# Kernel optimization log

Measured on AMD Instinct MI355X. Metric: run time of the kernel, lower is better.

Reference implementation:

```python
import jax, jax.numpy as jnp
import numpy as np

D_MODEL = 1024
NUM_HEADS = 16
D_K = D_MODEL // NUM_HEADS


def setup_inputs() -> dict:
    key = jax.random.key(0)
    ks = jax.random.split(key, 11)
    B, T = 4, 2048
    s = 1.0 / np.sqrt(D_MODEL)
    inp = {
        "query": jax.random.normal(ks[0], (B, T, D_MODEL), jnp.float32),
        "key": jax.random.normal(ks[1], (B, T, D_MODEL), jnp.float32),
        "value": jax.random.normal(ks[2], (B, T, D_MODEL), jnp.float32),
        "Wq": jax.random.uniform(ks[3], (D_MODEL, D_MODEL), jnp.float32, -s, s),
        "bq": jax.random.uniform(ks[4], (D_MODEL,), jnp.float32, -s, s),
        "Wk": jax.random.uniform(ks[5], (D_MODEL, D_MODEL), jnp.float32, -s, s),
        "bk": jax.random.uniform(ks[6], (D_MODEL,), jnp.float32, -s, s),
        "Wv": jax.random.uniform(ks[7], (D_MODEL, D_MODEL), jnp.float32, -s, s),
        "bv": jax.random.uniform(ks[8], (D_MODEL,), jnp.float32, -s, s),
        "Wo": jax.random.uniform(ks[9], (D_MODEL, D_MODEL), jnp.float32, -s, s),
        "bo": jax.random.uniform(ks[10], (D_MODEL,), jnp.float32, -s, s),
    }
    return inp


def _split_heads(x):
    B, T, _ = x.shape
    return x.reshape(B, T, NUM_HEADS, D_K).transpose(0, 2, 1, 3)  # (B,H,T,dk)


def reference(query, key, value, Wq, bq, Wk, bk, Wv, bv, Wo, bo):
    q = _split_heads(query @ Wq + bq)   # (B,H,Tq,dk)
    k = _split_heads(key @ Wk + bk)     # (B,H,Tk,dk)
    v = _split_heads(value @ Wv + bv)   # (B,H,Tk,dk)
    scale = 1.0 / jnp.sqrt(jnp.asarray(D_K, q.dtype))
    scores = jnp.einsum("bhqd,bhkd->bhqk", q, k) * scale
    weights = jax.nn.softmax(scores, axis=-1)
    attn = jnp.einsum("bhqk,bhkd->bhqd", weights, v)  # (B,H,Tq,dk)
    B, H, T, dk = attn.shape
    attn = attn.transpose(0, 2, 1, 3).reshape(B, T, H * dk)
    return attn @ Wo + bo
```

## Files before the change

kernel.cpp:

```cpp
#include <hip/hip_runtime.h>
#include <hip/hip_bf16.h>
#include <stdint.h>


typedef __bf16 bf16x8 __attribute__((ext_vector_type(8)));
typedef short  v4s    __attribute__((ext_vector_type(4)));
typedef float  f32x4  __attribute__((ext_vector_type(4)));

#define LOG2E 1.44269504088896340736f

static __device__ __forceinline__ uint32_t f2bf(float x) {
  uint32_t u = __float_as_uint(x);
  u += 0x7fffu + ((u >> 16) & 1u);
  return u >> 16;
}
#if __has_builtin(__builtin_amdgcn_cvt_pk_bf16_f32)
static __device__ __forceinline__ uint32_t pk2bf(float a, float b) {
  typedef __bf16 b2 __attribute__((ext_vector_type(2)));
  union { b2 v; uint32_t u; } x;
  x.v = __builtin_amdgcn_cvt_pk_bf16_f32(a, b);
  return x.u;
}
#else
static __device__ __forceinline__ uint32_t pk2bf(float a, float b) {
  return f2bf(a) | (f2bf(b) << 16);
}
#endif
static __device__ __forceinline__ void gl2lds16(const void* g, void* l) {
  __builtin_amdgcn_global_load_lds(
      (const __attribute__((address_space(1))) uint32_t*)g,
      (__attribute__((address_space(3))) uint32_t*)l, 16, 0, 0);
}

__global__ void convert_inputs(const float* __restrict__ q, const float* __restrict__ k,
                               const float* __restrict__ v, uint16_t* __restrict__ qo,
                               uint16_t* __restrict__ ko, uint16_t* __restrict__ vo) {
  const float* src = blockIdx.y == 0 ? q : (blockIdx.y == 1 ? k : v);
  uint16_t*    dst = blockIdx.y == 0 ? qo : (blockIdx.y == 1 ? ko : vo);
  size_t idx = ((size_t)blockIdx.x * 256 + threadIdx.x) * 8;
  float4 a = *(const float4*)(src + idx);
  float4 b = *(const float4*)(src + idx + 4);
  uint4 o;
  o.x = pk2bf(a.x, a.y); o.y = pk2bf(a.z, a.w);
  o.z = pk2bf(b.x, b.y); o.w = pk2bf(b.z, b.w);
  *(uint4*)(dst + idx) = o;
}

__global__ void transpose_weights(const float* __restrict__ Wq, const float* __restrict__ Wk,
                                  const float* __restrict__ Wv, const float* __restrict__ Wo,
                                  uint16_t* __restrict__ out) {
  __shared__ float t[32][33];
  const float* W = blockIdx.z == 0 ? Wq : blockIdx.z == 1 ? Wk : blockIdx.z == 2 ? Wv : Wo;
  uint16_t* O = out + (size_t)blockIdx.z * 1048576;
  int tx = threadIdx.x & 31, ty = threadIdx.x >> 5;
  int r0 = blockIdx.y * 32, c0 = blockIdx.x * 32;
#pragma unroll
  for (int i = 0; i < 4; i++) t[ty + i * 8][tx] = W[(size_t)(r0 + ty + i * 8) * 1024 + c0 + tx];
  __syncthreads();
#pragma unroll
  for (int i = 0; i < 4; i++)
    O[(size_t)(c0 + ty + i * 8) * 1024 + r0 + tx] = (uint16_t)f2bf(t[tx][ty + i * 8]);
}

static __device__ __forceinline__ void gemm_body(
    const uint16_t* __restrict__ A, const uint16_t* __restrict__ Bt,
    const float* __restrict__ bias, void* __restrict__ Cout,
    int N, int K, int mode, float oscale, int mBase, int nBase,
    uint16_t* __restrict__ lA, uint16_t* __restrict__ lB) {
  int tid = threadIdx.x, wave = tid >> 6, lane = tid & 63;
  int q = lane >> 4, c = lane & 15;
  int wrow = wave & 1, wcol = wave >> 1;
  f32x4 acc[4][4] = {};

  int swz = ((lane & 7) ^ (lane >> 3)) * 8;
  const uint16_t* gA = A + (size_t)(mBase + wave * 32 + (lane >> 3)) * K + swz;
  const uint16_t* gB = Bt + (size_t)(nBase + wave * 32 + (lane >> 3)) * K + swz;
  int cs = c & 7;

  for (int kt = 0; kt < K / 64; kt++) {
    __syncthreads();
    int k0 = kt * 64;
#pragma unroll
    for (int it = 0; it < 4; it++) {
      gl2lds16(gA + (size_t)(it * 8) * K + k0, &lA[(wave * 32 + it * 8) * 64]);
      gl2lds16(gB + (size_t)(it * 8) * K + k0, &lB[(wave * 32 + it * 8) * 64]);
    }
    __syncthreads();
#pragma unroll
    for (int kk = 0; kk < 2; kk++) {
      bf16x8 af[4], bfr[4];
#pragma unroll
      for (int i = 0; i < 4; i++)
        af[i] = *(const bf16x8*)&lA[(wrow * 64 + i * 16 + c) * 64 + ((kk * 4 + q) ^ cs) * 8];
#pragma unroll
      for (int j = 0; j < 4; j++)
        bfr[j] = *(const bf16x8*)&lB[(wcol * 64 + j * 16 + c) * 64 + ((kk * 4 + q) ^ cs) * 8];
#pragma unroll
      for (int i = 0; i < 4; i++)
#pragma unroll
        for (int j = 0; j < 4; j++)
          acc[i][j] = __builtin_amdgcn_mfma_f32_16x16x32_bf16(af[i], bfr[j], acc[i][j], 0, 0, 0);
    }
  }

  float bb[4];
#pragma unroll
  for (int j = 0; j < 4; j++) bb[j] = bias[nBase + wcol * 64 + j * 16 + c];

  if (mode == 0) {
    float* Co = (float*)Cout;
#pragma unroll
    for (int i = 0; i < 4; i++)
#pragma unroll
      for (int j = 0; j < 4; j++) {
        int row = mBase + wrow * 64 + i * 16 + q * 4;
        int col = nBase + wcol * 64 + j * 16 + c;
#pragma unroll
        for (int r = 0; r < 4; r++) Co[(size_t)(row + r) * N + col] = acc[i][j][r] + bb[j];
      }
  } else if (mode == 1) {
    uint16_t* Co = (uint16_t*)Cout;
#pragma unroll
    for (int i = 0; i < 4; i++)
#pragma unroll
      for (int j = 0; j < 4; j++) {
        int row = mBase + wrow * 64 + i * 16 + q * 4;
        int col = nBase + wcol * 64 + j * 16 + c;
#pragma unroll
        for (int r = 0; r < 4; r++)
          Co[(size_t)(row + r) * N + col] = (uint16_t)f2bf((acc[i][j][r] + bb[j]) * oscale);
      }
  } else {
    uint16_t* Co = (uint16_t*)Cout;
#pragma unroll
    for (int i = 0; i < 4; i++)
#pragma unroll
      for (int j = 0; j < 4; j++) {
        int n = nBase + wcol * 64 + j * 16 + c;
        int h = n >> 6, d = n & 63;
        int m = mBase + wrow * 64 + i * 16 + q * 4;
        int b = m >> 11, t = m & 2047;
        uint32_t lo = pk2bf(acc[i][j][0] + bb[j], acc[i][j][1] + bb[j]);
        uint32_t hi = pk2bf(acc[i][j][2] + bb[j], acc[i][j][3] + bb[j]);
        *(uint2*)(Co + (size_t)((b * 16 + h) * 64 + d) * 2048 + t) = make_uint2(lo, hi);
      }
  }
}

__global__ __launch_bounds__(256, 2)
void gemm_qkv(const uint16_t* __restrict__ qb, const uint16_t* __restrict__ kb,
              const uint16_t* __restrict__ vb, const uint16_t* __restrict__ Wtq,
              const uint16_t* __restrict__ Wtk, const uint16_t* __restrict__ Wtv,
              const float* __restrict__ bq, const float* __restrict__ bk,
              const float* __restrict__ bv, uint16_t* __restrict__ Qp,
              uint16_t* __restrict__ Kp, uint16_t* __restrict__ Vt, float cs) {
  __shared__ uint16_t lA[8192], lB[8192];
  int z = blockIdx.z;
  const uint16_t* A  = z == 0 ? qb : (z == 1 ? kb : vb);
  const uint16_t* Bt = z == 0 ? Wtq : (z == 1 ? Wtk : Wtv);
  const float* bias  = z == 0 ? bq : (z == 1 ? bk : bv);
  void* C            = z == 0 ? (void*)Qp : (z == 1 ? (void*)Kp : (void*)Vt);
  int mode   = z == 2 ? 2 : 1;
  float os   = z == 0 ? cs : 1.0f;
  gemm_body(A, Bt, bias, C, 1024, 1024, mode, os, blockIdx.y * 128, blockIdx.x * 128, lA, lB);
}

__global__ __launch_bounds__(256, 2)
void gemm_out(const uint16_t* __restrict__ A, const uint16_t* __restrict__ Bt,
              const float* __restrict__ bias, float* __restrict__ C) {
  __shared__ uint16_t lA[8192], lB[8192];
  gemm_body(A, Bt, bias, C, 1024, 1024, 0, 1.0f, blockIdx.y * 128, blockIdx.x * 128, lA, lB);
}

__global__ __launch_bounds__(256, 2)
void attn(const uint16_t* __restrict__ Qp, const uint16_t* __restrict__ Kp,
          const uint16_t* __restrict__ Vt, uint16_t* __restrict__ Ob) {
  __shared__ uint16_t lds[16384];
  int tid = threadIdx.x, wave = tid >> 6, lane = tid & 63;
  int q = lane >> 4, c = lane & 15;
  int cs = c & 7;

  int id = blockIdx.y * 16 + blockIdx.x;
  int wk = (id & 7) * 128 + (id >> 3);
  int qt = wk & 15, bh = wk >> 4;
  int b = bh >> 4, h = bh & 15;
  int qbase = qt * 128;
  int swz = ((lane & 7) ^ (lane >> 3)) * 8;

  {
    const uint16_t* gQ =
        Qp + (size_t)(b * 2048 + qbase + wave * 32 + (lane >> 3)) * 1024 + h * 64 + swz;
#pragma unroll
    for (int it = 0; it < 4; it++)
      gl2lds16(gQ + (size_t)(it * 8) * 1024, &lds[(wave * 32 + it * 8) * 64]);
  }
  __syncthreads();
  bf16x8 qf[2][2];
#pragma unroll
  for (int it = 0; it < 2; it++)
#pragma unroll
    for (int kk = 0; kk < 2; kk++)
      qf[it][kk] =
          *(const bf16x8*)&lds[(wave * 32 + it * 16 + c) * 64 + ((kk * 4 + q) ^ cs) * 8];
  __syncthreads();

  f32x4 o[4][2] = {};
  float rs0 = 0.f, rs1 = 0.f;

  const uint16_t* gK0 =
      Kp + (size_t)(b * 2048 + wave * 16 + (lane >> 3)) * 1024 + h * 64 + swz;
  const uint16_t* gV0 = Vt + (size_t)(bh * 64 + wave * 16 + (lane >> 3)) * 2048 + swz;

#pragma unroll
  for (int it = 0; it < 2; it++) {
    gl2lds16(gK0 + (size_t)(it * 8) * 1024, &lds[(wave * 16 + it * 8) * 64]);
    gl2lds16(gV0 + (size_t)(it * 8) * 2048, &lds[8192 + (wave * 16 + it * 8) * 64]);
  }

  for (int kt = 0; kt < 32; kt++) {
    int cur = kt & 1;
    __syncthreads();

    if (kt < 31) {
      int nb = (cur ^ 1) * 4096;
#pragma unroll
      for (int it = 0; it < 2; it++) {
        gl2lds16(gK0 + (size_t)((kt + 1) * 64 + it * 8) * 1024,
                 &lds[nb + (wave * 16 + it * 8) * 64]);
        gl2lds16(gV0 + (size_t)(it * 8) * 2048 + (kt + 1) * 64,
                 &lds[8192 + nb + (wave * 16 + it * 8) * 64]);
      }
    }

    const uint16_t* sKc = &lds[cur * 4096];
    const uint16_t* sVc = &lds[8192 + cur * 4096];

#pragma unroll
    for (int jt = 0; jt < 4; jt++) {
      bf16x8 a0 = *(const bf16x8*)&sKc[(jt * 16 + c) * 64 + (q ^ cs) * 8];
      bf16x8 a1 = *(const bf16x8*)&sKc[(jt * 16 + c) * 64 + ((4 + q) ^ cs) * 8];
      f32x4 s0 = __builtin_amdgcn_mfma_f32_16x16x32_bf16(a0, qf[0][0],
                                                         (f32x4){0.f, 0.f, 0.f, 0.f}, 0, 0, 0);
      s0 = __builtin_amdgcn_mfma_f32_16x16x32_bf16(a1, qf[0][1], s0, 0, 0, 0);
      f32x4 s1 = __builtin_amdgcn_mfma_f32_16x16x32_bf16(a0, qf[1][0],
                                                         (f32x4){0.f, 0.f, 0.f, 0.f}, 0, 0, 0);
      s1 = __builtin_amdgcn_mfma_f32_16x16x32_bf16(a1, qf[1][1], s1, 0, 0, 0);

      float p00 = __builtin_amdgcn_exp2f(s0[0]), p01 = __builtin_amdgcn_exp2f(s0[1]);
      float p02 = __builtin_amdgcn_exp2f(s0[2]), p03 = __builtin_amdgcn_exp2f(s0[3]);
      float p10 = __builtin_amdgcn_exp2f(s1[0]), p11 = __builtin_amdgcn_exp2f(s1[1]);
      float p12 = __builtin_amdgcn_exp2f(s1[2]), p13 = __builtin_amdgcn_exp2f(s1[3]);
      rs0 += (p00 + p01) + (p02 + p03);
      rs1 += (p10 + p11) + (p12 + p13);
      union { uint32_t u[2]; v4s s4; } pb0, pb1;
      pb0.u[0] = pk2bf(p00, p01); pb0.u[1] = pk2bf(p02, p03);
      pb1.u[0] = pk2bf(p10, p11); pb1.u[1] = pk2bf(p12, p13);

#pragma unroll
      for (int mt = 0; mt < 4; mt++) {
        v4s a = *(const v4s*)&sVc[(mt * 16 + c) * 64 + (((jt * 2 + (q >> 1)) ^ cs) * 8) +
                                  (q & 1) * 4];
        o[mt][0] = __builtin_amdgcn_mfma_f32_16x16x16bf16_1k(a, pb0.s4, o[mt][0], 0, 0, 0);
        o[mt][1] = __builtin_amdgcn_mfma_f32_16x16x16bf16_1k(a, pb1.s4, o[mt][1], 0, 0, 0);
      }
    }
  }

  rs0 += __shfl_xor(rs0, 16); rs0 += __shfl_xor(rs0, 32);
  rs1 += __shfl_xor(rs1, 16); rs1 += __shfl_xor(rs1, 32);
  float l[2] = {rs0, rs1};

#pragma unroll
  for (int it = 0; it < 2; it++) {
    float inv = 1.0f / l[it];
    size_t trow = (size_t)(b * 2048 + qbase + wave * 32 + it * 16 + c) * 1024 + h * 64;
#pragma unroll
    for (int mt = 0; mt < 4; mt++) {
      uint32_t lo = pk2bf(o[mt][it][0] * inv, o[mt][it][1] * inv);
      uint32_t hi = pk2bf(o[mt][it][2] * inv, o[mt][it][3] * inv);
      *(uint2*)(Ob + trow + mt * 16 + q * 4) = make_uint2(lo, hi);
    }
  }
}

extern "C" void kernel_launch(void* const* d_in, const int* in_sizes, int n_in,
                              void* d_out, int out_size, void* d_ws, size_t ws_size,
                              hipStream_t stream) {
  (void)in_sizes; (void)n_in; (void)out_size; (void)ws_size;
  const float* query = (const float*)d_in[0];
  const float* key_  = (const float*)d_in[1];
  const float* value = (const float*)d_in[2];
  const float* Wq = (const float*)d_in[3]; const float* bq = (const float*)d_in[4];
  const float* Wk = (const float*)d_in[5]; const float* bk = (const float*)d_in[6];
  const float* Wv = (const float*)d_in[7]; const float* bv = (const float*)d_in[8];
  const float* Wo = (const float*)d_in[9]; const float* bo = (const float*)d_in[10];

  const size_t SZ = (size_t)8192 * 1024;
  uint16_t* buf0 = (uint16_t*)d_ws;
  uint16_t* buf1 = buf0 + SZ;
  uint16_t* buf2 = buf1 + SZ;
  uint16_t* buf3 = buf2 + SZ;
  uint16_t* wts  = buf3 + SZ;
  uint16_t* Wtq = wts;
  uint16_t* Wtk = wts + 1048576;
  uint16_t* Wtv = wts + 2097152;
  uint16_t* Wto = wts + 3145728;
  uint16_t* Kp  = wts + 4194304;
  uint16_t* Vt  = Kp + SZ;

  const float Cs = 0.125f * LOG2E;

  convert_inputs<<<dim3(4096, 3), 256, 0, stream>>>(query, key_, value, buf0, buf1, buf2);
  transpose_weights<<<dim3(32, 32, 4), 256, 0, stream>>>(Wq, Wk, Wv, Wo, wts);
  gemm_qkv<<<dim3(8, 64, 3), 256, 0, stream>>>(buf0, buf1, buf2, Wtq, Wtk, Wtv,
                                               bq, bk, bv, buf3, Kp, Vt, Cs);
  attn<<<dim3(16, 64), 256, 0, stream>>>(buf3, Kp, Vt, buf2);
  gemm_out<<<dim3(8, 64), 256, 0, stream>>>(buf2, Wto, bo, (float*)d_out);
}
```

Baseline: 355.1 us.

## Widen attention blocks to 256 queries, XCD-swizzle GEMM tiles, add MFMA priority hints

The attention kernel now runs 512-thread blocks covering 256 query rows, so each K/V tile loaded into LDS is shared by twice as many queries. Each wave now loads only 8 rows per K/V tile. Both GEMM kernels remap block indices so neighbouring row tiles land on the same XCD, to improve L2 reuse of the A operand. s_setprio is raised around the MFMA sections of the attention inner loop so matrix work from one wave can overlap exp and convert work from others. The tighter launch bound of 512 threads with 4 blocks per CU lowers the per-thread register budget, which may cause spills in the attention kernel.

```diff
diff --git a/kernel.cpp b/kernel.cpp
--- a/kernel.cpp
+++ b/kernel.cpp
@@ -155,24 +155,32 @@
               const float* __restrict__ bv, uint16_t* __restrict__ Qp,
               uint16_t* __restrict__ Kp, uint16_t* __restrict__ Vt, float cs) {
   __shared__ uint16_t lA[8192], lB[8192];
-  int z = blockIdx.z;
+  int id = blockIdx.x + (blockIdx.y << 3) + (blockIdx.z << 9);
+  int xcd = id & 7, j = id >> 3;
+  int by = xcd * 8 + (j & 7);
+  int bx = (j >> 3) & 7;
+  int z  = j >> 6;
   const uint16_t* A  = z == 0 ? qb : (z == 1 ? kb : vb);
   const uint16_t* Bt = z == 0 ? Wtq : (z == 1 ? Wtk : Wtv);
   const float* bias  = z == 0 ? bq : (z == 1 ? bk : bv);
   void* C            = z == 0 ? (void*)Qp : (z == 1 ? (void*)Kp : (void*)Vt);
   int mode   = z == 2 ? 2 : 1;
   float os   = z == 0 ? cs : 1.0f;
-  gemm_body(A, Bt, bias, C, 1024, 1024, mode, os, blockIdx.y * 128, blockIdx.x * 128, lA, lB);
+  gemm_body(A, Bt, bias, C, 1024, 1024, mode, os, by * 128, bx * 128, lA, lB);
 }
 
 __global__ __launch_bounds__(256, 2)
 void gemm_out(const uint16_t* __restrict__ A, const uint16_t* __restrict__ Bt,
               const float* __restrict__ bias, float* __restrict__ C) {
   __shared__ uint16_t lA[8192], lB[8192];
-  gemm_body(A, Bt, bias, C, 1024, 1024, 0, 1.0f, blockIdx.y * 128, blockIdx.x * 128, lA, lB);
-}
-
-__global__ __launch_bounds__(256, 2)
+  int id = blockIdx.x + (blockIdx.y << 3);
+  int xcd = id & 7, j = id >> 3;
+  int by = xcd * 8 + (j & 7);
+  int bx = j >> 3;
+  gemm_body(A, Bt, bias, C, 1024, 1024, 0, 1.0f, by * 128, bx * 128, lA, lB);
+}
+
+__global__ __launch_bounds__(512, 4)
 void attn(const uint16_t* __restrict__ Qp, const uint16_t* __restrict__ Kp,
           const uint16_t* __restrict__ Vt, uint16_t* __restrict__ Ob) {
   __shared__ uint16_t lds[16384];
@@ -180,11 +188,11 @@
   int q = lane >> 4, c = lane & 15;
   int cs = c & 7;
 
-  int id = blockIdx.y * 16 + blockIdx.x;
-  int wk = (id & 7) * 128 + (id >> 3);
-  int qt = wk & 15, bh = wk >> 4;
+  int id = blockIdx.y * 8 + blockIdx.x;
+  int wk = (id & 7) * 64 + (id >> 3);
+  int qt = wk & 7, bh = wk >> 3;
   int b = bh >> 4, h = bh & 15;
-  int qbase = qt * 128;
+  int qbase = qt * 256;
   int swz = ((lane & 7) ^ (lane >> 3)) * 8;
 
   {
@@ -208,14 +216,11 @@
   float rs0 = 0.f, rs1 = 0.f;
 
   const uint16_t* gK0 =
-      Kp + (size_t)(b * 2048 + wave * 16 + (lane >> 3)) * 1024 + h * 64 + swz;
-  const uint16_t* gV0 = Vt + (size_t)(bh * 64 + wave * 16 + (lane >> 3)) * 2048 + swz;
-
-#pragma unroll
-  for (int it = 0; it < 2; it++) {
-    gl2lds16(gK0 + (size_t)(it * 8) * 1024, &lds[(wave * 16 + it * 8) * 64]);
-    gl2lds16(gV0 + (size_t)(it * 8) * 2048, &lds[8192 + (wave * 16 + it * 8) * 64]);
-  }
+      Kp + (size_t)(b * 2048 + wave * 8 + (lane >> 3)) * 1024 + h * 64 + swz;
+  const uint16_t* gV0 = Vt + (size_t)(bh * 64 + wave * 8 + (lane >> 3)) * 2048 + swz;
+
+  gl2lds16(gK0, &lds[(wave * 8) * 64]);
+  gl2lds16(gV0, &lds[8192 + (wave * 8) * 64]);
 
   for (int kt = 0; kt < 32; kt++) {
     int cur = kt & 1;
@@ -223,13 +228,8 @@
 
     if (kt < 31) {
       int nb = (cur ^ 1) * 4096;
-#pragma unroll
-      for (int it = 0; it < 2; it++) {
-        gl2lds16(gK0 + (size_t)((kt + 1) * 64 + it * 8) * 1024,
-                 &lds[nb + (wave * 16 + it * 8) * 64]);
-        gl2lds16(gV0 + (size_t)(it * 8) * 2048 + (kt + 1) * 64,
-                 &lds[8192 + nb + (wave * 16 + it * 8) * 64]);
-      }
+      gl2lds16(gK0 + (size_t)(kt + 1) * 64 * 1024, &lds[nb + (wave * 8) * 64]);
+      gl2lds16(gV0 + (size_t)(kt + 1) * 64, &lds[8192 + nb + (wave * 8) * 64]);
     }
 
     const uint16_t* sKc = &lds[cur * 4096];
@@ -239,12 +239,14 @@
     for (int jt = 0; jt < 4; jt++) {
       bf16x8 a0 = *(const bf16x8*)&sKc[(jt * 16 + c) * 64 + (q ^ cs) * 8];
       bf16x8 a1 = *(const bf16x8*)&sKc[(jt * 16 + c) * 64 + ((4 + q) ^ cs) * 8];
+      __builtin_amdgcn_s_setprio(1);
       f32x4 s0 = __builtin_amdgcn_mfma_f32_16x16x32_bf16(a0, qf[0][0],
                                                          (f32x4){0.f, 0.f, 0.f, 0.f}, 0, 0, 0);
       s0 = __builtin_amdgcn_mfma_f32_16x16x32_bf16(a1, qf[0][1], s0, 0, 0, 0);
       f32x4 s1 = __builtin_amdgcn_mfma_f32_16x16x32_bf16(a0, qf[1][0],
                                                          (f32x4){0.f, 0.f, 0.f, 0.f}, 0, 0, 0);
       s1 = __builtin_amdgcn_mfma_f32_16x16x32_bf16(a1, qf[1][1], s1, 0, 0, 0);
+      __builtin_amdgcn_s_setprio(0);
 
       float p00 = __builtin_amdgcn_exp2f(s0[0]), p01 = __builtin_amdgcn_exp2f(s0[1]);
       float p02 = __builtin_amdgcn_exp2f(s0[2]), p03 = __builtin_amdgcn_exp2f(s0[3]);
@@ -256,6 +258,7 @@
       pb0.u[0] = pk2bf(p00, p01); pb0.u[1] = pk2bf(p02, p03);
       pb1.u[0] = pk2bf(p10, p11); pb1.u[1] = pk2bf(p12, p13);
 
+      __builtin_amdgcn_s_setprio(1);
 #pragma unroll
       for (int mt = 0; mt < 4; mt++) {
         v4s a = *(const v4s*)&sVc[(mt * 16 + c) * 64 + (((jt * 2 + (q >> 1)) ^ cs) * 8) +
@@ -263,6 +266,7 @@
         o[mt][0] = __builtin_amdgcn_mfma_f32_16x16x16bf16_1k(a, pb0.s4, o[mt][0], 0, 0, 0);
         o[mt][1] = __builtin_amdgcn_mfma_f32_16x16x16bf16_1k(a, pb1.s4, o[mt][1], 0, 0, 0);
       }
+      __builtin_amdgcn_s_setprio(0);
     }
   }
 
@@ -314,6 +318,6 @@
   transpose_weights<<<dim3(32, 32, 4), 256, 0, stream>>>(Wq, Wk, Wv, Wo, wts);
   gemm_qkv<<<dim3(8, 64, 3), 256, 0, stream>>>(buf0, buf1, buf2, Wtq, Wtk, Wtv,
                                                bq, bk, bv, buf3, Kp, Vt, Cs);
-  attn<<<dim3(16, 64), 256, 0, stream>>>(buf3, Kp, Vt, buf2);
+  attn<<<dim3(8, 64), 512, 0, stream>>>(buf3, Kp, Vt, buf2);
   gemm_out<<<dim3(8, 64), 256, 0, stream>>>(buf2, Wto, bo, (float*)d_out);
 }
```

Measured after the change: 356.0 us. Within noise of the previous version (+0.2%).
